# Performance work log

Measured on AMD Instinct MI355X. Metric: run time of the kernel, lower is better.

Reference implementation:

```python
import jax, jax.numpy as jnp
import numpy as np

D_MODEL, D_STATE, D_CONV, EXPAND = 1024, 16, 4, 2
D_INNER = EXPAND * D_MODEL  # 2048
DT_RANK = (D_MODEL + 15) // 16  # 64
BATCH, SEQ = 2, 2048


def setup_inputs() -> dict:
    key = jax.random.key(0)
    ks = jax.random.split(key, 8)
    s = 0.02
    A = jnp.tile(jnp.arange(1, D_STATE + 1, dtype=jnp.float32), (D_INNER, 1))
    return {
        "x": jax.random.normal(ks[0], (BATCH, SEQ, D_MODEL), jnp.float32),
        "in_proj_w": jax.random.normal(ks[1], (D_MODEL, 2 * D_INNER), jnp.float32) * s,
        "conv_w": jax.random.normal(ks[2], (D_INNER, 1, D_CONV), jnp.float32) * s,
        "conv_b": jnp.zeros((D_INNER,), jnp.float32),
        "x_proj_w": jax.random.normal(ks[3], (D_INNER, DT_RANK + 2 * D_STATE), jnp.float32) * s,
        "dt_proj_w": jax.random.normal(ks[4], (DT_RANK, D_INNER), jnp.float32) * s,
        "dt_proj_b": jnp.zeros((D_INNER,), jnp.float32),
        "A_log": jnp.log(A),
        "D": jnp.ones((D_INNER,), jnp.float32),
        "out_proj_w": jax.random.normal(ks[5], (D_INNER, D_MODEL), jnp.float32) * s,
    }


def _mamba(x, in_proj_w, conv_w, conv_b, x_proj_w, dt_proj_w, dt_proj_b, A_log, D, out_proj_w):
    d_inner, d_state = A_log.shape
    dt_rank = dt_proj_w.shape[0]
    seq_len = x.shape[1]

    xr = x @ in_proj_w                       # (B, L, 2*ED)
    xb, res = jnp.split(xr, 2, axis=-1)      # each (B, L, ED)

    # causal depthwise conv1d (torch pads both sides then truncates to seq_len
    # == left-pad-only causal conv)
    xc = jnp.swapaxes(xb, 1, 2)              # (B, ED, L)
    xc = jax.lax.conv_general_dilated(
        xc, conv_w, window_strides=(1,),
        padding=[(conv_w.shape[-1] - 1, 0)],
        dimension_numbers=("NCH", "OIH", "NCH"),
        feature_group_count=d_inner)
    xc = xc + conv_b[None, :, None]
    u = jax.nn.silu(jnp.swapaxes(xc, 1, 2))  # (B, L, ED)

    dbc = u @ x_proj_w                       # (B, L, dt_rank + 2*N)
    dt, Bc, Cc = jnp.split(dbc, [dt_rank, dt_rank + d_state], axis=-1)
    dt = jax.nn.softplus(dt @ dt_proj_w + dt_proj_b)  # (B, L, ED)
    A = -jnp.exp(A_log)                      # (ED, N)

    def step(h, xs):
        dt_i, B_i, C_i, u_i = xs             # (B,ED), (B,N), (B,N), (B,ED)
        dA = jnp.exp(dt_i[:, :, None] * A)   # (B, ED, N)
        h = h * dA + (dt_i * u_i)[:, :, None] * B_i[:, None, :]
        y = jnp.einsum("bdn,bn->bd", h, C_i) + D * u_i
        return h, y

    h0 = jnp.zeros((x.shape[0], d_inner, d_state), x.dtype)
    xs = (jnp.swapaxes(dt, 0, 1), jnp.swapaxes(Bc, 0, 1),
          jnp.swapaxes(Cc, 0, 1), jnp.swapaxes(u, 0, 1))
    _, ys = jax.lax.scan(step, h0, xs)       # ys: (L, B, ED)
    y_ssm = jnp.swapaxes(ys, 0, 1)           # (B, L, ED)

    y = y_ssm * jax.nn.silu(res)
    return y @ out_proj_w                    # (B, L, d_model)


def reference(x, in_proj_w, conv_w, conv_b, x_proj_w, dt_proj_w, dt_proj_b, A_log, D, out_proj_w):
    return _mamba(x, in_proj_w, conv_w, conv_b, x_proj_w, dt_proj_w, dt_proj_b, A_log, D, out_proj_w)
```

## Files before the change

kernel.cpp:

```cpp
#include <hip/hip_runtime.h>
#include <cstddef>
#include <cstdint>

#define BATCH 2
#define SEQ   2048
#define DM    1024
#define ED    2048
#define NS    16
#define DR    64
#define NROWS (BATCH*SEQ)

#define NCHUNK 32
#define CLEN   64
#define CSTATES (BATCH*ED*NS)

#define OFF_XBH   ((size_t)0)
#define OFF_RESH  ((size_t)4194304)
#define OFF_PS    ((size_t)8388608)
#define OFF_DT    ((size_t)12582912)
#define OFF_DBC   ((size_t)16777216)
#define OFF_WT    ((size_t)17170432)

typedef _Float16 half8 __attribute__((ext_vector_type(8)));
typedef _Float16 half4 __attribute__((ext_vector_type(4)));
typedef float    floatx4 __attribute__((ext_vector_type(4)));

__device__ __forceinline__ float silu_f(float x) { return x / (1.f + __expf(-x)); }

__device__ __forceinline__ void gload_lds16(const _Float16* g, _Float16* l) {
  __builtin_amdgcn_global_load_lds(
      (const __attribute__((address_space(1))) void*)g,
      (__attribute__((address_space(3))) void*)l, 16, 0, 0);
}

template<int BN, int WGM, int WGN, int EPI, int BK>
__global__ __launch_bounds__(256)
void hgemm(const _Float16* __restrict__ A, int lda,
           const _Float16* __restrict__ Bt, int ldb,
           float* __restrict__ C, _Float16* __restrict__ Ch,
           _Float16* __restrict__ Ch2, int N, int K) {
  constexpr int BM = 128;
  constexpr int FM = BM / 16 / WGM;
  constexpr int FN = BN / 16 / WGN;
  constexpr int CPR = BK / 8;
  __shared__ _Float16 sA[BM * BK];
  __shared__ _Float16 sB[BN * BK];
  const int tid = threadIdx.x;
  const int ln  = tid & 63;
  const int wid = tid >> 6;
  const int wm  = wid % WGM;
  const int wn  = wid / WGM;
  const int m0  = blockIdx.y * BM;
  const int n0  = blockIdx.x * BN;
  const int l15 = ln & 15;
  const int q   = ln >> 4;

  floatx4 acc[FM][FN];
  #pragma unroll
  for (int i = 0; i < FM; ++i)
    #pragma unroll
    for (int j = 0; j < FN; ++j)
      acc[i][j] = floatx4{0.f, 0.f, 0.f, 0.f};

  for (int k0 = 0; k0 < K; k0 += BK) {
    __syncthreads();
    #pragma unroll
    for (int s = 0; s < (BM * CPR) / 256; ++s) {
      const int i = s * 256 + tid;
      const int m = i / CPR;
      const int cg = (i & (CPR - 1)) ^ ((m >> 1) & (CPR - 1));
      gload_lds16(A + (size_t)(m0 + m) * lda + k0 + cg * 8, sA + i * 8);
    }
    #pragma unroll
    for (int s = 0; s < (BN * CPR) / 256; ++s) {
      const int i = s * 256 + tid;
      const int n = i / CPR;
      const int cg = (i & (CPR - 1)) ^ ((n >> 1) & (CPR - 1));
      gload_lds16(Bt + (size_t)(n0 + n) * ldb + k0 + cg * 8, sB + i * 8);
    }
    __syncthreads();

    #pragma unroll
    for (int h = 0; h < BK / 32; ++h) {
      half8 af[FM], bf[FN];
      #pragma unroll
      for (int fm = 0; fm < FM; ++fm) {
        const int mr = wm * FM * 16 + fm * 16 + l15;
        const int cl = (h * 4 + q) ^ ((mr >> 1) & (CPR - 1));
        af[fm] = *(const half8*)(sA + mr * BK + cl * 8);
      }
      #pragma unroll
      for (int fn = 0; fn < FN; ++fn) {
        const int nr = wn * FN * 16 + fn * 16 + l15;
        const int cl = (h * 4 + q) ^ ((nr >> 1) & (CPR - 1));
        bf[fn] = *(const half8*)(sB + nr * BK + cl * 8);
      }
      #pragma unroll
      for (int fm = 0; fm < FM; ++fm)
        #pragma unroll
        for (int fn = 0; fn < FN; ++fn)
          acc[fm][fn] = __builtin_amdgcn_mfma_f32_16x16x32_f16(
              af[fm], bf[fn], acc[fm][fn], 0, 0, 0);
    }
  }

  #pragma unroll
  for (int fm = 0; fm < FM; ++fm) {
    #pragma unroll
    for (int fn = 0; fn < FN; ++fn) {
      const int col = n0 + wn * FN * 16 + fn * 16 + l15;
      #pragma unroll
      for (int r = 0; r < 4; ++r) {
        const int row = m0 + wm * FM * 16 + fm * 16 + q * 4 + r;
        const float v = acc[fm][fn][r];
        if (EPI == 2) {
          if (col < ED) Ch[(size_t)row * ED + col] = (_Float16)v;
          else          Ch2[(size_t)row * ED + (col - ED)] = (_Float16)silu_f(v);
        } else {
          C[(size_t)row * N + col] = v;
        }
      }
    }
  }
}

__global__ __launch_bounds__(256)
void xproj_conv_kernel(const _Float16* __restrict__ xbh,
                       const float* __restrict__ convw,
                       const float* __restrict__ convb,
                       const _Float16* __restrict__ Wxt,
                       float* __restrict__ dbc) {
  constexpr int BM = 128, BN = 96, BK = 64, CPR = 8;
  __shared__ _Float16 sA[BM * BK];
  __shared__ _Float16 sB[BN * BK];
  const int tid = threadIdx.x;
  const int ln  = tid & 63;
  const int wid = tid >> 6;
  const int m0  = blockIdx.x * BM;
  const int l15 = ln & 15;
  const int q   = ln >> 4;
  const int kbeg = blockIdx.y * (ED / 8);

  floatx4 acc[2][6];
  #pragma unroll
  for (int i = 0; i < 2; ++i)
    #pragma unroll
    for (int j = 0; j < 6; ++j) acc[i][j] = floatx4{0.f, 0.f, 0.f, 0.f};

  for (int k0 = kbeg; k0 < kbeg + ED / 8; k0 += BK) {
    __syncthreads();
    #pragma unroll
    for (int s = 0; s < (BM * CPR) / 256; ++s) {
      const int i = s * 256 + tid;
      const int m = i / CPR;
      const int cg = (i & (CPR - 1)) ^ ((m >> 1) & (CPR - 1));
      const int r = m0 + m;
      const int t = r & (SEQ - 1);
      const int ch = k0 + cg * 8;
      const _Float16* xp = xbh + (size_t)r * ED + ch;
      const half8 v0 = *(const half8*)(xp);
      half8 v1 = {}, v2 = {}, v3 = {};
      if (t >= 1) v1 = *(const half8*)(xp - ED);
      if (t >= 2) v2 = *(const half8*)(xp - 2 * ED);
      if (t >= 3) v3 = *(const half8*)(xp - 3 * ED);
      half8 o;
      #pragma unroll
      for (int j = 0; j < 8; ++j) {
        const float4 wv = ((const float4*)convw)[ch + j];
        float a = convb[ch + j];
        a = fmaf(wv.w, (float)v0[j], a);
        a = fmaf(wv.z, (float)v1[j], a);
        a = fmaf(wv.y, (float)v2[j], a);
        a = fmaf(wv.x, (float)v3[j], a);
        o[j] = (_Float16)silu_f(a);
      }
      *(half8*)(sA + i * 8) = o;
    }
    #pragma unroll
    for (int s = 0; s < 3; ++s) {
      const int i = s * 256 + tid;
      const int n = i / CPR;
      const int cg = (i & (CPR - 1)) ^ ((n >> 1) & (CPR - 1));
      gload_lds16(Wxt + (size_t)n * ED + k0 + cg * 8, sB + i * 8);
    }
    __syncthreads();

    #pragma unroll
    for (int h = 0; h < 2; ++h) {
      half8 af[2], bf[6];
      #pragma unroll
      for (int fm = 0; fm < 2; ++fm) {
        const int mr = wid * 32 + fm * 16 + l15;
        const int cl = (h * 4 + q) ^ ((mr >> 1) & (CPR - 1));
        af[fm] = *(const half8*)(sA + mr * BK + cl * 8);
      }
      #pragma unroll
      for (int fn = 0; fn < 6; ++fn) {
        const int nr = fn * 16 + l15;
        const int cl = (h * 4 + q) ^ ((nr >> 1) & (CPR - 1));
        bf[fn] = *(const half8*)(sB + nr * BK + cl * 8);
      }
      #pragma unroll
      for (int fm = 0; fm < 2; ++fm)
        #pragma unroll
        for (int fn = 0; fn < 6; ++fn)
          acc[fm][fn] = __builtin_amdgcn_mfma_f32_16x16x32_f16(
              af[fm], bf[fn], acc[fm][fn], 0, 0, 0);
    }
  }

  #pragma unroll
  for (int fm = 0; fm < 2; ++fm) {
    #pragma unroll
    for (int fn = 0; fn < 6; ++fn) {
      const int col = fn * 16 + l15;
      #pragma unroll
      for (int r = 0; r < 4; ++r) {
        const int row = m0 + wid * 32 + fm * 16 + q * 4 + r;
        unsafeAtomicAdd(&dbc[(size_t)row * 96 + col], acc[fm][fn][r]);
      }
    }
  }
}

__global__ __launch_bounds__(256)
void dt_kernel(const float* __restrict__ dbc, const _Float16* __restrict__ Wdtt,
               const float* __restrict__ bdt, _Float16* __restrict__ dth) {
  constexpr int BM = 128, BN = 128, BK = 64, CPR = 8;
  __shared__ _Float16 sA[BM * BK];
  __shared__ _Float16 sB[BN * BK];
  const int tid = threadIdx.x;
  const int ln  = tid & 63;
  const int wid = tid >> 6;
  const int wm  = wid & 1;
  const int wn  = wid >> 1;
  const int m0  = blockIdx.y * BM;
  const int n0  = blockIdx.x * BN;
  const int l15 = ln & 15;
  const int q   = ln >> 4;

  #pragma unroll
  for (int s = 0; s < 4; ++s) {
    const int i = s * 256 + tid;
    const int m = i / CPR;
    const int cg = (i & (CPR - 1)) ^ ((m >> 1) & (CPR - 1));
    const float* p = dbc + (size_t)(m0 + m) * 96 + cg * 8;
    const float4 a = *(const float4*)(p);
    const float4 b = *(const float4*)(p + 4);
    half8 o;
    o[0] = (_Float16)a.x; o[1] = (_Float16)a.y; o[2] = (_Float16)a.z; o[3] = (_Float16)a.w;
    o[4] = (_Float16)b.x; o[5] = (_Float16)b.y; o[6] = (_Float16)b.z; o[7] = (_Float16)b.w;
    *(half8*)(sA + i * 8) = o;
  }
  #pragma unroll
  for (int s = 0; s < 4; ++s) {
    const int i = s * 256 + tid;
    const int n = i / CPR;
    const int cg = (i & (CPR - 1)) ^ ((n >> 1) & (CPR - 1));
    gload_lds16(Wdtt + (size_t)(n0 + n) * DR + cg * 8, sB + i * 8);
  }
  __syncthreads();

  floatx4 acc[4][4];
  #pragma unroll
  for (int i = 0; i < 4; ++i)
    #pragma unroll
    for (int j = 0; j < 4; ++j) acc[i][j] = floatx4{0.f, 0.f, 0.f, 0.f};

  #pragma unroll
  for (int h = 0; h < 2; ++h) {
    half8 af[4], bf[4];
    #pragma unroll
    for (int fm = 0; fm < 4; ++fm) {
      const int mr = wm * 64 + fm * 16 + l15;
      const int cl = (h * 4 + q) ^ ((mr >> 1) & (CPR - 1));
      af[fm] = *(const half8*)(sA + mr * BK + cl * 8);
    }
    #pragma unroll
    for (int fn = 0; fn < 4; ++fn) {
      const int nr = wn * 64 + fn * 16 + l15;
      const int cl = (h * 4 + q) ^ ((nr >> 1) & (CPR - 1));
      bf[fn] = *(const half8*)(sB + nr * BK + cl * 8);
    }
    #pragma unroll
    for (int fm = 0; fm < 4; ++fm)
      #pragma unroll
      for (int fn = 0; fn < 4; ++fn)
        acc[fm][fn] = __builtin_amdgcn_mfma_f32_16x16x32_f16(
            af[fm], bf[fn], acc[fm][fn], 0, 0, 0);
  }

  #pragma unroll
  for (int fm = 0; fm < 4; ++fm) {
    #pragma unroll
    for (int fn = 0; fn < 4; ++fn) {
      const int col = n0 + wn * 64 + fn * 16 + l15;
      #pragma unroll
      for (int r = 0; r < 4; ++r) {
        const int row = m0 + wm * 64 + fm * 16 + q * 4 + r;
        float v = acc[fm][fn][r] + bdt[col];
        v = fmaxf(v, 0.f) + log1pf(__expf(-fabsf(v)));
        dth[(size_t)row * ED + col] = (_Float16)v;
      }
    }
  }
}

__device__ __forceinline__ void transpose_tile(const float* __restrict__ src,
                                               _Float16* __restrict__ dst,
                                               int R, int C, int bx, int by,
                                               int tid) {
  __shared__ float t[32][33];
  const int tx = tid & 31, ty = tid >> 5;
  const int c0 = bx * 32, r0 = by * 32;
  #pragma unroll
  for (int s = 0; s < 4; ++s)
    t[ty + s * 8][tx] = src[(size_t)(r0 + ty + s * 8) * C + c0 + tx];
  __syncthreads();
  #pragma unroll
  for (int s = 0; s < 4; ++s)
    dst[(size_t)(c0 + ty + s * 8) * R + r0 + tx] = (_Float16)t[tx][ty + s * 8];
}

#define PREP_BLOCKS 10944
__global__ __launch_bounds__(256)
void prep_kernel(const float* __restrict__ x, _Float16* __restrict__ x_h,
                 const float* __restrict__ Win, _Float16* __restrict__ Wint,
                 const float* __restrict__ Wout, _Float16* __restrict__ Woutt,
                 const float* __restrict__ Wx, _Float16* __restrict__ Wxt,
                 const float* __restrict__ Wdt, _Float16* __restrict__ Wdtt,
                 float* __restrict__ dbc) {
  const int bid = blockIdx.x, tid = threadIdx.x;
  if (bid < 4096) {
    const int i = bid * 1024 + tid * 4;
    const float4 v = *(const float4*)(x + i);
    half4 o;
    o[0] = (_Float16)v.x; o[1] = (_Float16)v.y;
    o[2] = (_Float16)v.z; o[3] = (_Float16)v.w;
    *(half4*)(x_h + i) = o;
  } else if (bid < 8192) {
    const int t = bid - 4096;
    transpose_tile(Win, Wint, DM, 2 * ED, t & 127, t >> 7, tid);
  } else if (bid < 10240) {
    const int t = bid - 8192;
    transpose_tile(Wout, Woutt, ED, DM, t & 31, t >> 5, tid);
  } else if (bid < 10432) {
    const int t = bid - 10240;
    transpose_tile(Wx, Wxt, ED, 96, t % 3, t / 3, tid);
  } else if (bid < 10560) {
    const int t = bid - 10432;
    transpose_tile(Wdt, Wdtt, DR, ED, t & 63, t >> 6, tid);
  } else {
    const int i = (bid - 10560) * 1024 + tid * 4;
    *(float4*)(dbc + i) = float4{0.f, 0.f, 0.f, 0.f};
  }
}

__device__ __forceinline__ void conv_init_h(const _Float16* xbp, int tg0,
                                            float& x1, float& x2, float& x3) {
  x1 = (tg0 >= 1) ? (float)xbp[-(int)ED] : 0.f;
  x2 = (tg0 >= 2) ? (float)xbp[-2 * (int)ED] : 0.f;
  x3 = (tg0 >= 3) ? (float)xbp[-3 * (int)ED] : 0.f;
}

__global__ __launch_bounds__(256)
void scan2_summary(const _Float16* __restrict__ dth, const _Float16* __restrict__ xbh,
                   const float* __restrict__ convw, const float* __restrict__ convb,
                   const float* __restrict__ dbc, const float* __restrict__ A_log,
                   float* __restrict__ Pbuf, float* __restrict__ Sbuf) {
  const int d = blockIdx.x * 256 + threadIdx.x;
  const int b = blockIdx.y;
  const int g = blockIdx.z;

  float Adn[16];
  {
    const float4* al = (const float4*)(A_log + (size_t)d * NS);
    #pragma unroll
    for (int i = 0; i < 4; ++i) {
      const float4 v = al[i];
      Adn[i * 4 + 0] = -__expf(v.x); Adn[i * 4 + 1] = -__expf(v.y);
      Adn[i * 4 + 2] = -__expf(v.z); Adn[i * 4 + 3] = -__expf(v.w);
    }
  }
  const float4 wv = ((const float4*)convw)[d];
  const float cbd = convb[d];

  float P[16], S[16];
  #pragma unroll
  for (int n = 0; n < 16; ++n) { P[n] = 1.f; S[n] = 0.f; }

  const int tg0 = g * CLEN;
  const size_t row0 = (size_t)b * SEQ + tg0;
  const _Float16* dtp = dth + row0 * ED + d;
  const _Float16* xbp = xbh + row0 * ED + d;
  float x1, x2, x3;
  conv_init_h(xbp, tg0, x1, x2, x3);

  for (int t = 0; t < CLEN; ++t) {
    const float xt  = (float)xbp[(size_t)t * ED];
    const float dti = (float)dtp[(size_t)t * ED];
    float cv = cbd;
    cv = fmaf(wv.w, xt, cv);
    cv = fmaf(wv.z, x1, cv);
    cv = fmaf(wv.y, x2, cv);
    cv = fmaf(wv.x, x3, cv);
    const float ui = silu_f(cv);
    x3 = x2; x2 = x1; x1 = xt;

    const float4* bc = (const float4*)(dbc + (row0 + t) * 96 + DR);
    float Bv[16];
    #pragma unroll
    for (int i = 0; i < 4; ++i) {
      const float4 v = bc[i];
      Bv[i * 4 + 0] = v.x; Bv[i * 4 + 1] = v.y;
      Bv[i * 4 + 2] = v.z; Bv[i * 4 + 3] = v.w;
    }
    const float dtu = dti * ui;
    #pragma unroll
    for (int n = 0; n < 16; ++n) {
      const float a = __expf(dti * Adn[n]);
      S[n] = fmaf(S[n], a, dtu * Bv[n]);
      P[n] *= a;
    }
  }
  const size_t c0 = (size_t)g * CSTATES + ((size_t)(b * ED + d)) * NS;
  #pragma unroll
  for (int i = 0; i < 4; ++i) {
    *(float4*)(Pbuf + c0 + i * 4) = float4{P[i*4], P[i*4+1], P[i*4+2], P[i*4+3]};
    *(float4*)(Sbuf + c0 + i * 4) = float4{S[i*4], S[i*4+1], S[i*4+2], S[i*4+3]};
  }
}

__global__ __launch_bounds__(256)
void scan2_compose(float* __restrict__ Pbuf, const float* __restrict__ Sbuf) {
  const unsigned c = blockIdx.x * 256 + threadIdx.x;
  float h = 0.f;
  for (int g = 0; g < NCHUNK; ++g) {
    const size_t idx = (size_t)g * CSTATES + c;
    const float p = Pbuf[idx], s = Sbuf[idx];
    Pbuf[idx] = h;
    h = fmaf(p, h, s);
  }
}

__global__ __launch_bounds__(256)
void scan2_apply(const _Float16* __restrict__ dth, const _Float16* __restrict__ xbh,
                 const float* __restrict__ convw, const float* __restrict__ convb,
                 const float* __restrict__ dbc, const float* __restrict__ A_log,
                 const float* __restrict__ Dp, const float* __restrict__ Pbuf,
                 _Float16* __restrict__ resh) {
  const int d = blockIdx.x * 256 + threadIdx.x;
  const int b = blockIdx.y;
  const int g = blockIdx.z;

  float Adn[16];
  {
    const float4* al = (const float4*)(A_log + (size_t)d * NS);
    #pragma unroll
    for (int i = 0; i < 4; ++i) {
      const float4 v = al[i];
      Adn[i * 4 + 0] = -__expf(v.x); Adn[i * 4 + 1] = -__expf(v.y);
      Adn[i * 4 + 2] = -__expf(v.z); Adn[i * 4 + 3] = -__expf(v.w);
    }
  }
  const float4 wv = ((const float4*)convw)[d];
  const float cbd = convb[d];
  const float Dd = Dp[d];

  float h[16];
  const size_t c0 = (size_t)g * CSTATES + ((size_t)(b * ED + d)) * NS;
  #pragma unroll
  for (int i = 0; i < 4; ++i) {
    const float4 v = *(const float4*)(Pbuf + c0 + i * 4);
    h[i * 4 + 0] = v.x; h[i * 4 + 1] = v.y;
    h[i * 4 + 2] = v.z; h[i * 4 + 3] = v.w;
  }

  const int tg0 = g * CLEN;
  const size_t row0 = (size_t)b * SEQ + tg0;
  const _Float16* dtp = dth + row0 * ED + d;
  const _Float16* xbp = xbh + row0 * ED + d;
  _Float16* rp = resh + row0 * ED + d;
  float x1, x2, x3;
  conv_init_h(xbp, tg0, x1, x2, x3);

  for (int t = 0; t < CLEN; ++t) {
    const float xt  = (float)xbp[(size_t)t * ED];
    const float dti = (float)dtp[(size_t)t * ED];
    float cv = cbd;
    cv = fmaf(wv.w, xt, cv);
    cv = fmaf(wv.z, x1, cv);
    cv = fmaf(wv.y, x2, cv);
    cv = fmaf(wv.x, x3, cv);
    const float ui = silu_f(cv);
    x3 = x2; x2 = x1; x1 = xt;

    const float4* bc = (const float4*)(dbc + (row0 + t) * 96 + DR);
    float Bv[16], Cv[16];
    #pragma unroll
    for (int i = 0; i < 4; ++i) {
      const float4 v = bc[i];
      Bv[i * 4 + 0] = v.x; Bv[i * 4 + 1] = v.y;
      Bv[i * 4 + 2] = v.z; Bv[i * 4 + 3] = v.w;
      const float4 w = bc[4 + i];
      Cv[i * 4 + 0] = w.x; Cv[i * 4 + 1] = w.y;
      Cv[i * 4 + 2] = w.z; Cv[i * 4 + 3] = w.w;
    }
    const float dtu = dti * ui;
    float y = Dd * ui;
    #pragma unroll
    for (int n = 0; n < 16; ++n) {
      const float a = __expf(dti * Adn[n]);
      h[n] = fmaf(h[n], a, dtu * Bv[n]);
      y = fmaf(h[n], Cv[n], y);
    }
    const float sres = (float)rp[(size_t)t * ED];
    rp[(size_t)t * ED] = (_Float16)(y * sres);
  }
}

extern "C" void kernel_launch(void* const* d_in, const int* in_sizes, int n_in,
                              void* d_out, int out_size, void* d_ws, size_t ws_size,
                              hipStream_t stream) {
  (void)in_sizes; (void)n_in; (void)out_size; (void)ws_size;
  const float* x     = (const float*)d_in[0];
  const float* Win   = (const float*)d_in[1];
  const float* convw = (const float*)d_in[2];
  const float* convb = (const float*)d_in[3];
  const float* Wx    = (const float*)d_in[4];
  const float* Wdt   = (const float*)d_in[5];
  const float* bdt   = (const float*)d_in[6];
  const float* Alog  = (const float*)d_in[7];
  const float* Dp    = (const float*)d_in[8];
  const float* Wout  = (const float*)d_in[9];

  float* ws   = (float*)d_ws;
  _Float16* xbh  = (_Float16*)(ws + OFF_XBH);
  _Float16* resh = (_Float16*)(ws + OFF_RESH);
  float* Pbuf = ws + OFF_PS;
  float* Sbuf = ws + OFF_PS + 2097152;
  _Float16* dth = (_Float16*)(ws + OFF_DT);
  float* dbc  = ws + OFF_DBC;
  _Float16* Woutt = (_Float16*)(ws + OFF_WT);
  _Float16* Wxt   = (_Float16*)(ws + OFF_WT + 1048576);
  _Float16* Wdtt  = (_Float16*)(ws + OFF_WT + 1146880);
  float* out  = (float*)d_out;

  _Float16* x_h  = (_Float16*)(ws + OFF_DT);
  _Float16* Wint = (_Float16*)(ws + OFF_DT + 2097152);

  prep_kernel<<<PREP_BLOCKS, 256, 0, stream>>>(
      x, x_h, Win, Wint, Wout, Woutt, Wx, Wxt, Wdt, Wdtt, dbc);
  hgemm<128, 2, 2, 2, 64><<<dim3((2 * ED) / 128, NROWS / 128), 256, 0, stream>>>(
      x_h, DM, Wint, DM, nullptr, xbh, resh, 2 * ED, DM);
  xproj_conv_kernel<<<dim3(NROWS / 128, 8), 256, 0, stream>>>(
      xbh, convw, convb, Wxt, dbc);
  dt_kernel<<<dim3(ED / 128, NROWS / 128), 256, 0, stream>>>(
      dbc, Wdtt, bdt, dth);
  scan2_summary<<<dim3(ED / 256, BATCH, NCHUNK), 256, 0, stream>>>(
      dth, xbh, convw, convb, dbc, Alog, Pbuf, Sbuf);
  scan2_compose<<<CSTATES / 256, 256, 0, stream>>>(Pbuf, Sbuf);
  scan2_apply<<<dim3(ED / 256, BATCH, NCHUNK), 256, 0, stream>>>(
      dth, xbh, convw, convb, dbc, Alog, Dp, Pbuf, resh);
  hgemm<64, 4, 1, 0, 64><<<dim3(DM / 64, NROWS / 128), 256, 0, stream>>>(
      resh, ED, Woutt, ED, out, nullptr, nullptr, DM, ED);
}
```

Measured before the change: 340.9 us.

## Widen transpose tiles, compute chunk decay via dt sum, retile out-proj GEMM

The prep kernel's weight transposes now use 64x32 tiles and write paired half2 stores, so fewer blocks are launched and global writes are wider. The scan summary kernel no longer keeps a running product of per-step decays. It accumulates the sum of dt and evaluates exp(A*sum) once at the end, which removes 16 multiplies per step and frees registers. The output projection GEMM changes from 64-wide to 128-wide N tiles with a 2x2 wave layout, trading grid size for more reuse per tile.

```diff
diff --git a/kernel.cpp b/kernel.cpp
--- a/kernel.cpp
+++ b/kernel.cpp
@@ -23,6 +23,7 @@
 
 typedef _Float16 half8 __attribute__((ext_vector_type(8)));
 typedef _Float16 half4 __attribute__((ext_vector_type(4)));
+typedef _Float16 half2v __attribute__((ext_vector_type(2)));
 typedef float    floatx4 __attribute__((ext_vector_type(4)));
 
 __device__ __forceinline__ float silu_f(float x) { return x / (1.f + __expf(-x)); }
@@ -306,23 +307,30 @@
   }
 }
 
-__device__ __forceinline__ void transpose_tile(const float* __restrict__ src,
-                                               _Float16* __restrict__ dst,
-                                               int R, int C, int bx, int by,
-                                               int tid) {
-  __shared__ float t[32][33];
+__device__ __forceinline__ void transpose_tile2(const float* __restrict__ src,
+                                                _Float16* __restrict__ dst,
+                                                int R, int C, int bx, int by,
+                                                int tid) {
+  __shared__ float t[64][33];
   const int tx = tid & 31, ty = tid >> 5;
-  const int c0 = bx * 32, r0 = by * 32;
-  #pragma unroll
-  for (int s = 0; s < 4; ++s)
+  const int c0 = bx * 32, r0 = by * 64;
+  #pragma unroll
+  for (int s = 0; s < 8; ++s)
     t[ty + s * 8][tx] = src[(size_t)(r0 + ty + s * 8) * C + c0 + tx];
   __syncthreads();
-  #pragma unroll
-  for (int s = 0; s < 4; ++s)
-    dst[(size_t)(c0 + ty + s * 8) * R + r0 + tx] = (_Float16)t[tx][ty + s * 8];
-}
-
-#define PREP_BLOCKS 10944
+  const int rr2 = tid & 31;
+  const int cc  = tid >> 5;
+  #pragma unroll
+  for (int s = 0; s < 4; ++s) {
+    const int row = cc + s * 8;
+    half2v o;
+    o[0] = (_Float16)t[2 * rr2 + 0][row];
+    o[1] = (_Float16)t[2 * rr2 + 1][row];
+    *(half2v*)(dst + (size_t)(c0 + row) * R + r0 + 2 * rr2) = o;
+  }
+}
+
+#define PREP_BLOCKS 7712
 __global__ __launch_bounds__(256)
 void prep_kernel(const float* __restrict__ x, _Float16* __restrict__ x_h,
                  const float* __restrict__ Win, _Float16* __restrict__ Wint,
@@ -338,20 +346,20 @@
     o[0] = (_Float16)v.x; o[1] = (_Float16)v.y;
     o[2] = (_Float16)v.z; o[3] = (_Float16)v.w;
     *(half4*)(x_h + i) = o;
-  } else if (bid < 8192) {
+  } else if (bid < 6144) {
     const int t = bid - 4096;
-    transpose_tile(Win, Wint, DM, 2 * ED, t & 127, t >> 7, tid);
-  } else if (bid < 10240) {
-    const int t = bid - 8192;
-    transpose_tile(Wout, Woutt, ED, DM, t & 31, t >> 5, tid);
-  } else if (bid < 10432) {
-    const int t = bid - 10240;
-    transpose_tile(Wx, Wxt, ED, 96, t % 3, t / 3, tid);
-  } else if (bid < 10560) {
-    const int t = bid - 10432;
-    transpose_tile(Wdt, Wdtt, DR, ED, t & 63, t >> 6, tid);
+    transpose_tile2(Win, Wint, DM, 2 * ED, t & 127, t >> 7, tid);
+  } else if (bid < 7168) {
+    const int t = bid - 6144;
+    transpose_tile2(Wout, Woutt, ED, DM, t & 31, t >> 5, tid);
+  } else if (bid < 7264) {
+    const int t = bid - 7168;
+    transpose_tile2(Wx, Wxt, ED, 96, t % 3, t / 3, tid);
+  } else if (bid < 7328) {
+    const int t = bid - 7264;
+    transpose_tile2(Wdt, Wdtt, DR, ED, t, 0, tid);
   } else {
-    const int i = (bid - 10560) * 1024 + tid * 4;
+    const int i = (bid - 7328) * 1024 + tid * 4;
     *(float4*)(dbc + i) = float4{0.f, 0.f, 0.f, 0.f};
   }
 }
@@ -385,9 +393,10 @@
   const float4 wv = ((const float4*)convw)[d];
   const float cbd = convb[d];
 
-  float P[16], S[16];
-  #pragma unroll
-  for (int n = 0; n < 16; ++n) { P[n] = 1.f; S[n] = 0.f; }
+  float S[16];
+  #pragma unroll
+  for (int n = 0; n < 16; ++n) S[n] = 0.f;
+  float dsum = 0.f;
 
   const int tg0 = g * CLEN;
   const size_t row0 = (size_t)b * SEQ + tg0;
@@ -406,6 +415,7 @@
     cv = fmaf(wv.x, x3, cv);
     const float ui = silu_f(cv);
     x3 = x2; x2 = x1; x1 = xt;
+    dsum += dti;
 
     const float4* bc = (const float4*)(dbc + (row0 + t) * 96 + DR);
     float Bv[16];
@@ -420,13 +430,17 @@
     for (int n = 0; n < 16; ++n) {
       const float a = __expf(dti * Adn[n]);
       S[n] = fmaf(S[n], a, dtu * Bv[n]);
-      P[n] *= a;
     }
   }
   const size_t c0 = (size_t)g * CSTATES + ((size_t)(b * ED + d)) * NS;
   #pragma unroll
   for (int i = 0; i < 4; ++i) {
-    *(float4*)(Pbuf + c0 + i * 4) = float4{P[i*4], P[i*4+1], P[i*4+2], P[i*4+3]};
+    float4 pv;
+    pv.x = __expf(Adn[i * 4 + 0] * dsum);
+    pv.y = __expf(Adn[i * 4 + 1] * dsum);
+    pv.z = __expf(Adn[i * 4 + 2] * dsum);
+    pv.w = __expf(Adn[i * 4 + 3] * dsum);
+    *(float4*)(Pbuf + c0 + i * 4) = pv;
     *(float4*)(Sbuf + c0 + i * 4) = float4{S[i*4], S[i*4+1], S[i*4+2], S[i*4+3]};
   }
 }
@@ -562,6 +576,6 @@
   scan2_compose<<<CSTATES / 256, 256, 0, stream>>>(Pbuf, Sbuf);
   scan2_apply<<<dim3(ED / 256, BATCH, NCHUNK), 256, 0, stream>>>(
       dth, xbh, convw, convb, dbc, Alog, Dp, Pbuf, resh);
-  hgemm<64, 4, 1, 0, 64><<<dim3(DM / 64, NROWS / 128), 256, 0, stream>>>(
+  hgemm<128, 2, 2, 0, 64><<<dim3(DM / 128, NROWS / 128), 256, 0, stream>>>(
       resh, ED, Woutt, ED, out, nullptr, nullptr, DM, ED);
 }
```

Result: no change. 344.9 us (+1.2%).
